# Kernel tuning notes

Measured on AMD Instinct MI355X. Metric: run time of the kernel, lower is better.

Reference implementation:

```python
import jax, jax.numpy as jnp
import numpy as np

B, CIN, T, H, W = 1, 256, 64, 32, 32
A, G = 8, 8
SCALES = jnp.array([1., 2., 4., 8., 16., 32., 64., 128.], dtype=jnp.float32)
FEAT_STRIDE = 8.0
NMS_TOP_N = 100
NMS_THRESH = 0.7
MIN_SIZE = 4.0
POS_THR, NEG_THR = 0.7, 0.3
NEG_INF = -1e9


def _conv3d(x, w, b, strides):
    y = jax.lax.conv_general_dilated(
        x, w, window_strides=strides, padding=[(1, 1)] * 3,
        dimension_numbers=('NCDHW', 'OIDHW', 'NCDHW'))
    return y + b[None, :, None, None, None]


def _iou(a, b):
    # 1D interval IoU; a, b broadcastable [..., 2] = (start, end)
    inter = jnp.maximum(jnp.minimum(a[..., 1], b[..., 1]) - jnp.maximum(a[..., 0], b[..., 0]), 0.0)
    union = (a[..., 1] - a[..., 0]) + (b[..., 1] - b[..., 0]) - inter
    return inter / jnp.maximum(union, 1e-6)


def _nms(boxes, scores):
    # greedy 1D NMS: boxes [N,2], scores [N] -> top NMS_TOP_N (zero-padded)
    n = scores.shape[0]
    def step(sc, _):
        i = jnp.argmax(sc)
        s, box = sc[i], boxes[i]
        sup = (_iou(box[None], boxes) > NMS_THRESH) | (jnp.arange(n) == i)
        return jnp.where(sup, NEG_INF, sc), (box, s)
    _, (kb, ks) = jax.lax.scan(step, scores, None, length=NMS_TOP_N)
    keep = ks > NEG_INF * 0.5
    return jnp.where(keep[:, None], kb, 0.0), jnp.where(keep, ks, 0.0)


def _forward(base_feat, gt_chunks, video_len, c1w, c1b, c2w, c2b, sw, sb, dw, db):
    bsz = base_feat.shape[0]
    x = _conv3d(base_feat, c1w, c1b, (1, 2, 2))
    x = _conv3d(x, c2w, c2b, (1, 2, 2))
    feat = jnp.max(x, axis=(3, 4))                       # AdaptiveMaxPool3d((None,1,1)) -> [B,512,T]
    tlen = feat.shape[2]
    score_logit = (jnp.einsum('oc,bct->bot', sw, feat) + sb[None, :, None]).reshape(bsz, 2, A, tlen)
    delta = (jnp.einsum('oc,bct->bot', dw, feat) + db[None, :, None]).reshape(bsz, 2, A, tlen)
    prob = jax.nn.softmax(score_logit, axis=1)
    logp = jax.nn.log_softmax(score_logit, axis=1)

    # anchors: A lengths x T temporal positions, flattened as a*T + t
    anchor_len = FEAT_STRIDE * SCALES                                    # [A]
    centers = (jnp.arange(tlen, dtype=jnp.float32) + 0.5) * FEAT_STRIDE  # [T]
    a_start = centers[None, :] - anchor_len[:, None] / 2                 # [A,T]
    a_end = centers[None, :] + anchor_len[:, None] / 2
    anchors = jnp.stack([a_start, a_end], -1).reshape(-1, 2)             # [N,2]
    N = A * tlen

    # ---- proposal decode + NMS ----
    dc, dl = delta[:, 0], delta[:, 1]                                    # [B,A,T]
    pc = centers[None, None, :] + dc * anchor_len[None, :, None]
    pl = anchor_len[None, :, None] * jnp.exp(jnp.clip(dl, -10.0, 10.0))
    lim = tlen * FEAT_STRIDE
    ps = jnp.clip(pc - pl / 2, 0.0, lim)
    pe = jnp.clip(pc + pl / 2, 0.0, lim)
    boxes = jnp.stack([ps, pe], -1).reshape(bsz, N, 2)
    fg = prob[:, 1].reshape(bsz, N)
    fg = jnp.where((pe - ps).reshape(bsz, N) >= MIN_SIZE, fg, NEG_INF)
    prop_coord, prop_score = jax.vmap(_nms)(boxes, fg)

    # ---- IoU-based label assignment ----
    ious = _iou(anchors[None, :, None, :], gt_chunks[:, None, :, :])     # [B,N,G]
    max_iou = ious.max(-1)
    arg = ious.argmax(-1)                                                # [B,N]
    label = jnp.where(max_iou < NEG_THR, 0, -1)
    label = jnp.where(max_iou >= POS_THR, 1, label)
    best = ious.argmax(1)                                                # best anchor per gt [B,G]
    bidx = jnp.arange(bsz)[:, None]
    label = label.at[bidx, best].set(1)
    vl = video_len.astype(jnp.float32)[:, None]
    inside = (anchors[None, :, 0] >= 0.0) & (anchors[None, :, 1] <= vl)
    label = jnp.where(inside, label, -1)

    matched = gt_chunks[bidx, arg]                                       # [B,N,2]
    gc = (matched[..., 0] + matched[..., 1]) / 2
    gl = jnp.maximum(matched[..., 1] - matched[..., 0], 1e-6)
    ac = (anchors[:, 0] + anchors[:, 1]) / 2
    al = anchors[:, 1] - anchors[:, 0]
    reg_label = jnp.stack([(gc - ac[None]) / al[None], jnp.log(gl / al[None])], -1)
    reg_label = jax.lax.stop_gradient(reg_label)                          # targets carry no grad

    # ---- losses ----
    logp2 = logp.reshape(bsz, 2, N).transpose(0, 2, 1)                   # [B,N,2]
    lab = jnp.maximum(label, 0)
    nll = -jnp.take_along_axis(logp2, lab[..., None], axis=2)[..., 0]
    mask = (label >= 0).astype(jnp.float32)
    cls_loss = (nll * mask).sum() / jnp.maximum(mask.sum(), 1.0)

    delta2 = delta.reshape(bsz, 2, N).transpose(0, 2, 1)                 # [B,N,2]
    d = delta2 - reg_label
    sl1 = jnp.where(jnp.abs(d) < 1.0, 0.5 * d * d, jnp.abs(d) - 0.5).sum(-1)
    pos = (label == 1).astype(jnp.float32)
    reg_loss = (sl1 * pos).sum() / jnp.maximum(pos.sum(), 1.0)
    return prop_coord, prop_score, cls_loss, reg_loss


def setup_inputs() -> dict:
    key = jax.random.key(0)
    ks = jax.random.split(key, 8)
    base_feat = jax.random.normal(ks[0], (B, CIN, T, H, W), jnp.float32)
    starts = jax.random.uniform(ks[1], (B, G), minval=0.0, maxval=448.0)
    lens = jax.random.uniform(ks[2], (B, G), minval=8.0, maxval=64.0)
    gt_chunks = jnp.stack([starts, jnp.clip(starts + lens, 0.0, T * FEAT_STRIDE)], -1)
    video_len = jnp.full((B,), int(T * FEAT_STRIDE), jnp.int32)
    s = 0.02
    return dict(
        base_feat=base_feat, gt_chunks=gt_chunks, video_len=video_len,
        conv1_w=jax.random.normal(ks[3], (512, CIN, 3, 3, 3), jnp.float32) * s,
        conv1_b=jnp.zeros((512,), jnp.float32),
        conv2_w=jax.random.normal(ks[4], (512, 512, 3, 3, 3), jnp.float32) * s,
        conv2_b=jnp.zeros((512,), jnp.float32),
        score_w=jax.random.normal(ks[5], (2 * A, 512), jnp.float32) * s,
        score_b=jnp.zeros((2 * A,), jnp.float32),
        delta_w=jax.random.normal(ks[6], (2 * A, 512), jnp.float32) * s,
        delta_b=jnp.zeros((2 * A,), jnp.float32),
    )


def reference(base_feat, gt_chunks, video_len, conv1_w, conv1_b, conv2_w, conv2_b, score_w, score_b, delta_w, delta_b):
    return _forward(base_feat, gt_chunks, video_len, conv1_w, conv1_b, conv2_w, conv2_b, score_w, score_b, delta_w, delta_b)
```

## Files before the change

kernel.cpp:

```cpp
#include <hip/hip_runtime.h>

typedef __attribute__((ext_vector_type(8))) _Float16 half8;
typedef __attribute__((ext_vector_type(4))) _Float16 half4;
typedef __attribute__((ext_vector_type(4))) float floatx4;

#define DI __device__ __forceinline__

DI void gl_lds16(const void* g, void* l) {
    __builtin_amdgcn_global_load_lds(
        (__attribute__((address_space(1))) void*)(g),
        (__attribute__((address_space(3))) void*)(l), 16, 0, 0);
}


__global__ __launch_bounds__(256) void prep_split(
        const float* __restrict__ w1, _Float16* __restrict__ w1I,
        const float* __restrict__ w2, _Float16* __restrict__ w2I,
        const float* __restrict__ in, _Float16* __restrict__ oI,
        float* __restrict__ zp) {
    __shared__ float L[13824];
    const int b = blockIdx.x;
    const int tid = threadIdx.x;
    if (b == 0 && tid < 64) zp[tid] = 0.0f;
    if (b < 512) {
        const float* src = w1 + (size_t)b * 6912;
        for (int idx = tid; idx < 6912; idx += 256) L[idx] = src[idx] * 64.0f;
        __syncthreads();
        for (int c = tid; c < 864; c += 256) {
            const int tap = c >> 5, o = c & 31;
            half8 h, l;
#pragma unroll
            for (int j = 0; j < 8; ++j) {
                const float x = L[(o * 8 + j) * 27 + tap];
                const _Float16 hh = (_Float16)x;
                h[j] = hh; l[j] = (_Float16)(x - (float)hh);
            }
            const size_t off = (size_t)b * 13824 + (size_t)(tap * 8 + (o >> 2)) * 64 + (o & 3) * 8;
            *(half8*)&w1I[off] = h;
            *(half8*)&w1I[off + 32] = l;
        }
    } else if (b < 1024) {
        const float* src = w2 + (size_t)(b - 512) * 13824;
        for (int idx = tid; idx < 13824; idx += 256) L[idx] = src[idx] * 64.0f;
        __syncthreads();
        for (int c = tid; c < 1728; c += 256) {
            const int tap = c >> 6, o = c & 63;
            half8 h, l;
#pragma unroll
            for (int j = 0; j < 8; ++j) {
                const float x = L[(o * 8 + j) * 27 + tap];
                const _Float16 hh = (_Float16)x;
                h[j] = hh; l[j] = (_Float16)(x - (float)hh);
            }
            const size_t off = (size_t)(b - 512) * 27648 + (size_t)(tap * 16 + (o >> 2)) * 64 + (o & 3) * 8;
            *(half8*)&w2I[off] = h;
            *(half8*)&w2I[off + 32] = l;
        }
    } else {
        const int idx = b - 1024;
        const int hb = idx & 1;
        const int s0 = (idx >> 1) * 64;
        const int cil = tid >> 1, part = tid & 1;
        const float* src = in + (size_t)(hb * 128 + cil) * 65536 + s0 + part * 32;
        float v[32];
#pragma unroll
        for (int q = 0; q < 8; ++q) *(float4*)(v + q * 4) = *(const float4*)(src + q * 4);
#pragma unroll
        for (int j = 0; j < 32; ++j) L[cil * 65 + part * 32 + j] = v[j];
        __syncthreads();
#pragma unroll
        for (int k = 0; k < 4; ++k) {
            const int c = tid + k * 256;
            const int sp = c >> 4, ol = c & 15;
            half8 h, l;
#pragma unroll
            for (int j = 0; j < 8; ++j) {
                const float x = L[(ol * 8 + j) * 65 + sp];
                const _Float16 hh = (_Float16)x;
                h[j] = hh; l[j] = (_Float16)(x - (float)hh);
            }
            const int og = hb * 16 + ol;
            const size_t off = (size_t)(s0 + sp) * 512 + (size_t)(og >> 2) * 64 + (og & 3) * 8;
            *(half8*)&oI[off] = h;
            *(half8*)&oI[off + 32] = l;
        }
    }
}

__global__ __launch_bounds__(256, 2) void conv1_mfma(
        const _Float16* __restrict__ xI, const _Float16* __restrict__ wI,
        const float* __restrict__ b1, const _Float16* __restrict__ zp,
        _Float16* __restrict__ yI) {
    __shared__ __align__(16) _Float16 A2[2][128 * 64];
    __shared__ __align__(16) _Float16 B3[3][128 * 64];
    const int tid = threadIdx.x;
    const int n_ = blockIdx.x;
    const int t = ((n_ & 7) << 3) | ((n_ >> 3) & 7);
    const int co_blk = (n_ >> 6) & 3;
    const int h0 = ((n_ >> 8) & 1) * 8;
    const int wid = tid >> 6, lane = tid & 63;
    const int wm = wid & 1, wn = wid >> 1;
    const int ml = lane & 15, ql = lane >> 4;
    const int cs0 = (ql ^ (ml & 7)) * 8;
    const int cs1 = ((4 + ql) ^ (ml & 7)) * 8;
    const int sl = lane & 7, rl = lane >> 3;
    const int lc = sl ^ rl;

    const _Float16* wA[4]; const _Float16* bB[4];
    int dstq[4]; bool hok[4], wok[4];
    const size_t wbo = (size_t)co_blk * 128 * 13824;
#pragma unroll
    for (int q = 0; q < 4; ++q) {
        const int row = (q * 4 + wid) * 8 + rl;
        wA[q] = wI + wbo + (size_t)row * 13824 + lc * 8;
        dstq[q] = (q * 4 + wid) * 512 + lane * 8;
        const int h = h0 + (row >> 4), w = row & 15;
        const int ih2 = 2 * h - 1, iw2 = 2 * w - 1;
        hok[q] = (ih2 >= 0); wok[q] = (iw2 >= 0);
        bB[q] = xI + (ptrdiff_t)(ih2 * 32 + iw2) * 512 + lc * 8;
    }
    const _Float16* zpl = zp + lc * 8;

    floatx4 zz = {0.f, 0.f, 0.f, 0.f};
    floatx4 acc[4][4];
#pragma unroll
    for (int i = 0; i < 4; ++i)
#pragma unroll
        for (int j = 0; j < 4; ++j) acc[i][j] = zz;

    auto stageA = [&](int kt, int cb, int KH, int KW, _Float16* Ad) {
        const size_t ab = (size_t)(((kt * 9 + KH * 3 + KW) * 8 + cb) * 64);
#pragma unroll
        for (int q = 0; q < 4; ++q) gl_lds16(wA[q] + ab, &Ad[dstq[q]]);
    };
    auto stageB = [&](int kt, int cb, int KH, int KW, _Float16* Bd) {
        const int it = t + kt - 1;
        const bool tok = ((unsigned)it < 64u);
        const ptrdiff_t boff = (ptrdiff_t)it * 524288 + KH * 16384 + KW * 512 + cb * 64;
#pragma unroll
        for (int q = 0; q < 4; ++q) {
            const bool ok = tok && (KH > 0 || hok[q]) && (KW > 0 || wok[q]);
            gl_lds16(ok ? (bB[q] + boff) : zpl, &Bd[dstq[q]]);
        }
    };

    stageA(0, 0, 0, 0, A2[0]);
    stageB(0, 0, 0, 0, B3[0]);
    stageB(0, 0, 0, 1, B3[1]);
    asm volatile("s_waitcnt vmcnt(4)" ::: "memory");
    __builtin_amdgcn_s_barrier();

    for (int o = 0; o < 24; ++o) {
        const int cb = o / 3, kt = o - cb * 3;
        const int o1 = o + 1;
        const int cb1 = o1 / 3, kt1 = o1 - cb1 * 3;
#pragma unroll
        for (int j = 0; j < 9; ++j) {
            const int par = (o + j) & 1;
            if (j < 8) stageA(kt, cb, (j + 1) / 3, (j + 1) % 3, A2[par ^ 1]);
            else       stageA(kt1, cb1, 0, 0, A2[par ^ 1]);
            if (j < 7)       stageB(kt, cb, (j + 2) / 3, (j + 2) % 3, B3[(j + 2) % 3]);
            else if (j == 7) stageB(kt1, cb1, 0, 0, B3[0]);
            else             stageB(kt1, cb1, 0, 1, B3[1]);

            const _Float16* Ab = A2[par];
            const _Float16* Bb = B3[j % 3];
            half8 ah[4], alo[4], bh8[4], blo[4];
#pragma unroll
            for (int mi = 0; mi < 4; ++mi) {
                ah[mi]  = *(const half8*)&Ab[(wm * 64 + mi * 16 + ml) * 64 + cs0];
                alo[mi] = *(const half8*)&Ab[(wm * 64 + mi * 16 + ml) * 64 + cs1];
            }
#pragma unroll
            for (int ni = 0; ni < 4; ++ni) {
                bh8[ni] = *(const half8*)&Bb[(wn * 64 + ni * 16 + ml) * 64 + cs0];
                blo[ni] = *(const half8*)&Bb[(wn * 64 + ni * 16 + ml) * 64 + cs1];
            }
            __builtin_amdgcn_s_setprio(1);
#pragma unroll
            for (int mi = 0; mi < 4; ++mi)
#pragma unroll
                for (int ni = 0; ni < 4; ++ni) {
                    acc[mi][ni] = __builtin_amdgcn_mfma_f32_16x16x32_f16(ah[mi],  bh8[ni], acc[mi][ni], 0, 0, 0);
                    acc[mi][ni] = __builtin_amdgcn_mfma_f32_16x16x32_f16(ah[mi],  blo[ni], acc[mi][ni], 0, 0, 0);
                    acc[mi][ni] = __builtin_amdgcn_mfma_f32_16x16x32_f16(alo[mi], bh8[ni], acc[mi][ni], 0, 0, 0);
                }
            __builtin_amdgcn_s_setprio(0);
            asm volatile("s_waitcnt vmcnt(4)" ::: "memory");
            __builtin_amdgcn_s_barrier();
        }
    }

    const int qr = ql * 4;
#pragma unroll
    for (int mi = 0; mi < 4; ++mi) {
        const int co = co_blk * 128 + wm * 64 + mi * 16 + qr;
#pragma unroll
        for (int ni = 0; ni < 4; ++ni) {
            const int n = wn * 64 + ni * 16 + ml;
            const int h = h0 + (n >> 4), w = n & 15;
            const size_t base = ((size_t)t * 256 + h * 16 + w) * 1024
                              + (size_t)(co >> 5) * 64 + (co & 31);
            half4 hv, lv;
#pragma unroll
            for (int r = 0; r < 4; ++r) {
                const float v = acc[mi][ni][r] * 0.015625f + b1[co + r];
                const _Float16 hb = (_Float16)v;
                hv[r] = hb;
                lv[r] = (_Float16)(v - (float)hb);
            }
            *(half4*)(yI + base) = hv;
            *(half4*)(yI + base + 32) = lv;
        }
    }
}

__global__ __launch_bounds__(256, 2) void conv2_mfma(
        const _Float16* __restrict__ xI, const _Float16* __restrict__ wI,
        const _Float16* __restrict__ zp,
        float* __restrict__ x2p) {
    __shared__ __align__(16) _Float16 A2[2][128 * 64];
    __shared__ __align__(16) _Float16 B3[3][128 * 64];
    const int tid = threadIdx.x;
    const int n_ = blockIdx.x;
    const int tp = ((n_ & 7) << 2) | ((n_ >> 3) & 3);
    const int co_blk = (n_ >> 5) & 3;
    const int ks = (n_ >> 7) & 3;
    const int wid = tid >> 6, lane = tid & 63;
    const int wm = wid & 1, wn = wid >> 1;
    const int ml = lane & 15, ql = lane >> 4;
    const int cs0 = (ql ^ (ml & 7)) * 8;
    const int cs1 = ((4 + ql) ^ (ml & 7)) * 8;
    const int sl = lane & 7, rl = lane >> 3;
    const int lc = sl ^ rl;

    const _Float16* wA[4]; const _Float16* bB[4];
    int dstq[4], itv[4]; bool hok[4], wok[4];
    const size_t wbo = (size_t)co_blk * 128 * 27648;
#pragma unroll
    for (int q = 0; q < 4; ++q) {
        const int row = (q * 4 + wid) * 8 + rl;
        wA[q] = wI + wbo + (size_t)row * 27648 + lc * 8;
        dstq[q] = (q * 4 + wid) * 512 + lane * 8;
        const int sp = row & 63;
        itv[q] = tp * 2 + (row >> 6) - 1;
        const int ih2 = 2 * (sp >> 3) - 1, iw2 = 2 * (sp & 7) - 1;
        hok[q] = (ih2 >= 0); wok[q] = (iw2 >= 0);
        bB[q] = xI + (ptrdiff_t)((itv[q] * 256 + ih2 * 16 + iw2) * 1024) + lc * 8;
    }
    const _Float16* zpl = zp + lc * 8;

    floatx4 zz = {0.f, 0.f, 0.f, 0.f};
    floatx4 acc[4][4];
#pragma unroll
    for (int i = 0; i < 4; ++i)
#pragma unroll
        for (int j = 0; j < 4; ++j) acc[i][j] = zz;

    auto stageA = [&](int kt, int cb, int KH, int KW, _Float16* Ad) {
        const size_t ab = (size_t)(((kt * 9 + KH * 3 + KW) * 16 + cb) * 64);
#pragma unroll
        for (int q = 0; q < 4; ++q) gl_lds16(wA[q] + ab, &Ad[dstq[q]]);
    };
    auto stageB = [&](int kt, int cb, int KH, int KW, _Float16* Bd) {
        const ptrdiff_t boff = (ptrdiff_t)kt * 262144 + KH * 16384 + KW * 1024 + cb * 64;
#pragma unroll
        for (int q = 0; q < 4; ++q) {
            const bool ok = ((unsigned)(itv[q] + kt) < 64u)
                         && (KH > 0 || hok[q]) && (KW > 0 || wok[q]);
            gl_lds16(ok ? (bB[q] + boff) : zpl, &Bd[dstq[q]]);
        }
    };

    stageA(0, ks * 4, 0, 0, A2[0]);
    stageB(0, ks * 4, 0, 0, B3[0]);
    stageB(0, ks * 4, 0, 1, B3[1]);
    asm volatile("s_waitcnt vmcnt(4)" ::: "memory");
    __builtin_amdgcn_s_barrier();

    for (int o = 0; o < 12; ++o) {
        const int kt = o % 3, cb = ks * 4 + o / 3;
        const int o1 = o + 1;
        const int kt1 = o1 % 3, cb1 = ks * 4 + o1 / 3;
#pragma unroll
        for (int j = 0; j < 9; ++j) {
            const int par = (o + j) & 1;
            if (j < 8) stageA(kt, cb, (j + 1) / 3, (j + 1) % 3, A2[par ^ 1]);
            else       stageA(kt1, cb1, 0, 0, A2[par ^ 1]);
            if (j < 7)       stageB(kt, cb, (j + 2) / 3, (j + 2) % 3, B3[(j + 2) % 3]);
            else if (j == 7) stageB(kt1, cb1, 0, 0, B3[0]);
            else             stageB(kt1, cb1, 0, 1, B3[1]);

            const _Float16* Ab = A2[par];
            const _Float16* Bb = B3[j % 3];
            half8 ah[4], alo[4], bh8[4], blo[4];
#pragma unroll
            for (int mi = 0; mi < 4; ++mi) {
                ah[mi]  = *(const half8*)&Ab[(wm * 64 + mi * 16 + ml) * 64 + cs0];
                alo[mi] = *(const half8*)&Ab[(wm * 64 + mi * 16 + ml) * 64 + cs1];
            }
#pragma unroll
            for (int ni = 0; ni < 4; ++ni) {
                bh8[ni] = *(const half8*)&Bb[(wn * 64 + ni * 16 + ml) * 64 + cs0];
                blo[ni] = *(const half8*)&Bb[(wn * 64 + ni * 16 + ml) * 64 + cs1];
            }
            __builtin_amdgcn_s_setprio(1);
#pragma unroll
            for (int mi = 0; mi < 4; ++mi)
#pragma unroll
                for (int ni = 0; ni < 4; ++ni) {
                    acc[mi][ni] = __builtin_amdgcn_mfma_f32_16x16x32_f16(ah[mi],  bh8[ni], acc[mi][ni], 0, 0, 0);
                    acc[mi][ni] = __builtin_amdgcn_mfma_f32_16x16x32_f16(ah[mi],  blo[ni], acc[mi][ni], 0, 0, 0);
                    acc[mi][ni] = __builtin_amdgcn_mfma_f32_16x16x32_f16(alo[mi], bh8[ni], acc[mi][ni], 0, 0, 0);
                }
            __builtin_amdgcn_s_setprio(0);
            asm volatile("s_waitcnt vmcnt(4)" ::: "memory");
            __builtin_amdgcn_s_barrier();
        }
    }

    const int qr = ql * 4;
#pragma unroll
    for (int mi = 0; mi < 4; ++mi) {
        const int co = co_blk * 128 + wm * 64 + mi * 16 + qr;
#pragma unroll
        for (int ni = 0; ni < 4; ++ni) {
            const int n = wn * 64 + ni * 16 + ml;
            const int ng = tp * 128 + n;
            float4 v;
            v.x = acc[mi][ni][0]; v.y = acc[mi][ni][1];
            v.z = acc[mi][ni][2]; v.w = acc[mi][ni][3];
            *(float4*)&x2p[((size_t)ks * 4096 + ng) * 512 + co] = v;
        }
    }
}

__global__ __launch_bounds__(256) void feat_head(
        const float* __restrict__ x2p, const float* __restrict__ b2,
        const float* __restrict__ sw, const float* __restrict__ sb,
        const float* __restrict__ dw, const float* __restrict__ db,
        float* __restrict__ scoreL, float* __restrict__ deltaL) {
    __shared__ float fr[512];
    __shared__ float partial[32][8];
    const int t = blockIdx.x, tid = threadIdx.x;
#pragma unroll
    for (int cc = 0; cc < 2; ++cc) {
        const int c = tid + cc * 256;
        float mx = -3.4e38f;
        for (int sp = 0; sp < 64; ++sp) {
            const size_t ng = (size_t)t * 64 + sp;
            const float s = x2p[ng * 512 + c]
                          + x2p[((size_t)4096 + ng) * 512 + c]
                          + x2p[((size_t)8192 + ng) * 512 + c]
                          + x2p[((size_t)12288 + ng) * 512 + c];
            mx = fmaxf(mx, s);
        }
        fr[c] = mx * 0.015625f + b2[c];
    }
    __syncthreads();
    const int o = tid & 31, part = tid >> 5;
    const float* wrow = (o < 16) ? (sw + (size_t)o * 512) : (dw + (size_t)(o - 16) * 512);
    float s = 0.f;
    const int j0 = part * 64;
#pragma unroll 16
    for (int j = 0; j < 64; ++j) s += wrow[j0 + j] * fr[j0 + j];
    partial[o][part] = s;
    __syncthreads();
    if (tid < 32) {
        float tot = 0.f;
#pragma unroll
        for (int p = 0; p < 8; ++p) tot += partial[tid][p];
        tot += (tid < 16) ? sb[tid] : db[tid - 16];
        if (tid < 16) scoreL[tid * 64 + t] = tot;
        else deltaL[(tid - 16) * 64 + t] = tot;
    }
}

__global__ void nms_loss_kernel(const float* __restrict__ scoreL,
                                const float* __restrict__ deltaL,
                                const float* __restrict__ gt,
                                const int* __restrict__ video_len,
                                float* __restrict__ out) {
    const int lane = threadIdx.x & 63;
    float gsv[8], gev[8];
#pragma unroll
    for (int g = 0; g < 8; ++g) { gsv[g] = gt[2 * g]; gev[g] = gt[2 * g + 1]; }
    const float center = ((float)lane + 0.5f) * 8.0f;
    float psv[8], pev[8], fg[8], l0v[8], l1v[8], dcv[8], dlv[8];
#pragma unroll
    for (int j = 0; j < 8; ++j) {
        const float s0 = scoreL[j * 64 + lane], s1 = scoreL[(8 + j) * 64 + lane];
        const float mm = fmaxf(s0, s1);
        const float lse = mm + logf(expf(s0 - mm) + expf(s1 - mm));
        l0v[j] = s0 - lse; l1v[j] = s1 - lse;
        const float dc = deltaL[j * 64 + lane], dl = deltaL[(8 + j) * 64 + lane];
        dcv[j] = dc; dlv[j] = dl;
        const float alen = 8.0f * (float)(1 << j);
        const float pc = center + dc * alen;
        const float pl = alen * expf(fminf(fmaxf(dl, -10.0f), 10.0f));
        const float ps = fminf(fmaxf(pc - pl * 0.5f, 0.0f), 512.0f);
        const float pe = fminf(fmaxf(pc + pl * 0.5f, 0.0f), 512.0f);
        psv[j] = ps; pev[j] = pe;
        fg[j] = ((pe - ps) >= 4.0f) ? expf(l1v[j]) : -1e9f;
    }
    for (int itn = 0; itn < 100; ++itn) {
        float v = fg[0]; int idx = lane;
#pragma unroll
        for (int j = 1; j < 8; ++j) if (fg[j] > v) { v = fg[j]; idx = lane + 64 * j; }
#pragma unroll
        for (int off = 32; off > 0; off >>= 1) {
            const float ov = __shfl_down(v, off);
            const int oi = __shfl_down(idx, off);
            if (ov > v || (ov == v && oi < idx)) { v = ov; idx = oi; }
        }
        v = __shfl(v, 0); idx = __shfl(idx, 0);
        const int wj = idx >> 6, wl = idx & 63;
        float bw0 = 0.f, bw1 = 0.f;
#pragma unroll
        for (int j = 0; j < 8; ++j) if (j == wj) { bw0 = psv[j]; bw1 = pev[j]; }
        const float b0 = __shfl(bw0, wl);
        const float b1 = __shfl(bw1, wl);
        if (lane == 0) {
            const bool kept = v > -5e8f;
            out[2 * itn] = kept ? b0 : 0.0f;
            out[2 * itn + 1] = kept ? b1 : 0.0f;
            out[200 + itn] = kept ? v : 0.0f;
        }
#pragma unroll
        for (int j = 0; j < 8; ++j) {
            const int n = lane + 64 * j;
            const float inter = fmaxf(fminf(b1, pev[j]) - fmaxf(b0, psv[j]), 0.0f);
            const float uni = (b1 - b0) + (pev[j] - psv[j]) - inter;
            const float iou = inter / fmaxf(uni, 1e-6f);
            if (iou > 0.7f || n == idx) fg[j] = -1e9f;
        }
    }
    int labv[8], aggv[8];
#pragma unroll
    for (int j = 0; j < 8; ++j) {
        const float alen = 8.0f * (float)(1 << j);
        const float as_ = center - alen * 0.5f, ae_ = center + alen * 0.5f;
        float mx = -1.0f; int ag = 0;
#pragma unroll
        for (int g = 0; g < 8; ++g) {
            const float inter = fmaxf(fminf(ae_, gev[g]) - fmaxf(as_, gsv[g]), 0.0f);
            const float uni = (ae_ - as_) + (gev[g] - gsv[g]) - inter;
            const float iou = inter / fmaxf(uni, 1e-6f);
            if (iou > mx) { mx = iou; ag = g; }
        }
        labv[j] = (mx < 0.3f) ? 0 : ((mx >= 0.7f) ? 1 : -1);
        aggv[j] = ag;
    }
    for (int g = 0; g < 8; ++g) {
        float v = -1.0f; int idx = 0;
#pragma unroll
        for (int j = 0; j < 8; ++j) {
            const int n = lane + 64 * j;
            const float alen = 8.0f * (float)(1 << j);
            const float as_ = center - alen * 0.5f, ae_ = center + alen * 0.5f;
            const float inter = fmaxf(fminf(ae_, gev[g]) - fmaxf(as_, gsv[g]), 0.0f);
            const float uni = (ae_ - as_) + (gev[g] - gsv[g]) - inter;
            const float iou = inter / fmaxf(uni, 1e-6f);
            if (iou > v || (iou == v && n < idx)) { v = iou; idx = n; }
        }
#pragma unroll
        for (int off = 32; off > 0; off >>= 1) {
            const float ov = __shfl_down(v, off);
            const int oi = __shfl_down(idx, off);
            if (ov > v || (ov == v && oi < idx)) { v = ov; idx = oi; }
        }
        idx = __shfl(idx, 0);
#pragma unroll
        for (int j = 0; j < 8; ++j)
            if (lane == (idx & 63) && j == (idx >> 6)) labv[j] = 1;
    }
    const float vl = (float)video_len[0];
    float nll_s = 0.f, msk_s = 0.f, reg_s = 0.f, pos_s = 0.f;
#pragma unroll
    for (int j = 0; j < 8; ++j) {
        const float alen = 8.0f * (float)(1 << j);
        const float as_ = center - alen * 0.5f, ae_ = center + alen * 0.5f;
        int l = labv[j];
        if (!((as_ >= 0.0f) && (ae_ <= vl))) l = -1;
        if (l >= 0) {
            msk_s += 1.0f;
            nll_s -= (l == 1) ? l1v[j] : l0v[j];
            if (l == 1) {
                pos_s += 1.0f;
                float gcv = 0.f, glv = 0.f;
#pragma unroll
                for (int g = 0; g < 8; ++g)
                    if (g == aggv[j]) {
                        gcv = (gsv[g] + gev[g]) * 0.5f;
                        glv = fmaxf(gev[g] - gsv[g], 1e-6f);
                    }
                const float r0 = (gcv - center) / alen;
                const float r1 = logf(glv / alen);
                const float d0 = dcv[j] - r0, d1 = dlv[j] - r1;
                float s = (fabsf(d0) < 1.0f) ? (0.5f * d0 * d0) : (fabsf(d0) - 0.5f);
                s += (fabsf(d1) < 1.0f) ? (0.5f * d1 * d1) : (fabsf(d1) - 0.5f);
                reg_s += s;
            }
        }
    }
    float sums[4] = {nll_s, msk_s, reg_s, pos_s};
#pragma unroll
    for (int k = 0; k < 4; ++k)
#pragma unroll
        for (int off = 32; off > 0; off >>= 1) sums[k] += __shfl_down(sums[k], off);
    if (lane == 0) {
        out[300] = sums[0] / fmaxf(sums[1], 1.0f);
        out[301] = sums[2] / fmaxf(sums[3], 1.0f);
    }
}

extern "C" void kernel_launch(void* const* d_in, const int* in_sizes, int n_in,
                              void* d_out, int out_size, void* d_ws, size_t ws_size,
                              hipStream_t stream) {
    const float* base_feat = (const float*)d_in[0];
    const float* gt        = (const float*)d_in[1];
    const int*   video_len = (const int*)d_in[2];
    const float* w1        = (const float*)d_in[3];
    const float* b1        = (const float*)d_in[4];
    const float* w2        = (const float*)d_in[5];
    const float* b2        = (const float*)d_in[6];
    const float* sw        = (const float*)d_in[7];
    const float* sb        = (const float*)d_in[8];
    const float* dw        = (const float*)d_in[9];
    const float* db        = (const float*)d_in[10];

    char* ws = (char*)d_ws;
    _Float16* w1I = (_Float16*)ws;  ws += (size_t)512 * 13824 * 2;
    _Float16* w2I = (_Float16*)ws;  ws += (size_t)512 * 27648 * 2;
    _Float16* inI = (_Float16*)ws;  ws += (size_t)65536 * 512 * 2;
    _Float16* x1I = (_Float16*)ws;  ws += (size_t)16384 * 1024 * 2;
    float* scoreL = (float*)ws;     ws += (size_t)16 * 64 * 4;
    float* deltaL = (float*)ws;     ws += (size_t)16 * 64 * 4;
    float* zpage  = (float*)ws;     ws += (size_t)64 * 4;
    float* x2p = (float*)inI;

    prep_split<<<3072, 256, 0, stream>>>(w1, w1I, w2, w2I, base_feat, inI, zpage);
    conv1_mfma<<<512, 256, 0, stream>>>(inI, w1I, b1,
                                        (const _Float16*)zpage, x1I);
    conv2_mfma<<<512, 256, 0, stream>>>(x1I, w2I,
                                        (const _Float16*)zpage, x2p);
    feat_head<<<64, 256, 0, stream>>>(x2p, b2, sw, sb, dw, db, scoreL, deltaL);
    nms_loss_kernel<<<1, 64, 0, stream>>>(scoreL, deltaL, gt, video_len,
                                          (float*)d_out);
}
```

Baseline: 750.7 us.

## Double-buffer B tile and prefetch B fragments into registers after barrier

Both conv kernels replace the triple-buffered B staging (two stages ahead) with a double buffer staged one step ahead, matching A. The B fragments for the next step are read from LDS into registers right after the barrier, so they are ready before the next MFMA block. This cuts LDS footprint (more room for occupancy) but the wait changes from vmcnt(4) to vmcnt(0). Each step now waits for all outstanding global-to-LDS loads, which reduces load/compute overlap and may expose memory latency.

```diff
diff --git a/kernel.cpp b/kernel.cpp
--- a/kernel.cpp
+++ b/kernel.cpp
@@ -92,7 +92,7 @@
         const float* __restrict__ b1, const _Float16* __restrict__ zp,
         _Float16* __restrict__ yI) {
     __shared__ __align__(16) _Float16 A2[2][128 * 64];
-    __shared__ __align__(16) _Float16 B3[3][128 * 64];
+    __shared__ __align__(16) _Float16 B2[2][128 * 64];
     const int tid = threadIdx.x;
     const int n_ = blockIdx.x;
     const int t = ((n_ & 7) << 3) | ((n_ >> 3) & 7);
@@ -144,11 +144,17 @@
         }
     };
 
+    half8 bh8c[4], bloc[4];
+
     stageA(0, 0, 0, 0, A2[0]);
-    stageB(0, 0, 0, 0, B3[0]);
-    stageB(0, 0, 0, 1, B3[1]);
-    asm volatile("s_waitcnt vmcnt(4)" ::: "memory");
+    stageB(0, 0, 0, 0, B2[0]);
+    asm volatile("s_waitcnt vmcnt(0)" ::: "memory");
     __builtin_amdgcn_s_barrier();
+#pragma unroll
+    for (int ni = 0; ni < 4; ++ni) {
+        bh8c[ni] = *(const half8*)&B2[0][(wn * 64 + ni * 16 + ml) * 64 + cs0];
+        bloc[ni] = *(const half8*)&B2[0][(wn * 64 + ni * 16 + ml) * 64 + cs1];
+    }
 
     for (int o = 0; o < 24; ++o) {
         const int cb = o / 3, kt = o - cb * 3;
@@ -157,37 +163,38 @@
 #pragma unroll
         for (int j = 0; j < 9; ++j) {
             const int par = (o + j) & 1;
-            if (j < 8) stageA(kt, cb, (j + 1) / 3, (j + 1) % 3, A2[par ^ 1]);
-            else       stageA(kt1, cb1, 0, 0, A2[par ^ 1]);
-            if (j < 7)       stageB(kt, cb, (j + 2) / 3, (j + 2) % 3, B3[(j + 2) % 3]);
-            else if (j == 7) stageB(kt1, cb1, 0, 0, B3[0]);
-            else             stageB(kt1, cb1, 0, 1, B3[1]);
-
+            if (j < 8) {
+                stageA(kt, cb, (j + 1) / 3, (j + 1) % 3, A2[par ^ 1]);
+                stageB(kt, cb, (j + 1) / 3, (j + 1) % 3, B2[par ^ 1]);
+            } else {
+                stageA(kt1, cb1, 0, 0, A2[par ^ 1]);
+                stageB(kt1, cb1, 0, 0, B2[par ^ 1]);
+            }
             const _Float16* Ab = A2[par];
-            const _Float16* Bb = B3[j % 3];
-            half8 ah[4], alo[4], bh8[4], blo[4];
+            half8 ah[4], alo[4];
 #pragma unroll
             for (int mi = 0; mi < 4; ++mi) {
                 ah[mi]  = *(const half8*)&Ab[(wm * 64 + mi * 16 + ml) * 64 + cs0];
                 alo[mi] = *(const half8*)&Ab[(wm * 64 + mi * 16 + ml) * 64 + cs1];
             }
-#pragma unroll
-            for (int ni = 0; ni < 4; ++ni) {
-                bh8[ni] = *(const half8*)&Bb[(wn * 64 + ni * 16 + ml) * 64 + cs0];
-                blo[ni] = *(const half8*)&Bb[(wn * 64 + ni * 16 + ml) * 64 + cs1];
-            }
             __builtin_amdgcn_s_setprio(1);
 #pragma unroll
             for (int mi = 0; mi < 4; ++mi)
 #pragma unroll
                 for (int ni = 0; ni < 4; ++ni) {
-                    acc[mi][ni] = __builtin_amdgcn_mfma_f32_16x16x32_f16(ah[mi],  bh8[ni], acc[mi][ni], 0, 0, 0);
-                    acc[mi][ni] = __builtin_amdgcn_mfma_f32_16x16x32_f16(ah[mi],  blo[ni], acc[mi][ni], 0, 0, 0);
-                    acc[mi][ni] = __builtin_amdgcn_mfma_f32_16x16x32_f16(alo[mi], bh8[ni], acc[mi][ni], 0, 0, 0);
+                    acc[mi][ni] = __builtin_amdgcn_mfma_f32_16x16x32_f16(ah[mi],  bh8c[ni], acc[mi][ni], 0, 0, 0);
+                    acc[mi][ni] = __builtin_amdgcn_mfma_f32_16x16x32_f16(ah[mi],  bloc[ni], acc[mi][ni], 0, 0, 0);
+                    acc[mi][ni] = __builtin_amdgcn_mfma_f32_16x16x32_f16(alo[mi], bh8c[ni], acc[mi][ni], 0, 0, 0);
                 }
             __builtin_amdgcn_s_setprio(0);
-            asm volatile("s_waitcnt vmcnt(4)" ::: "memory");
+            asm volatile("s_waitcnt vmcnt(0)" ::: "memory");
             __builtin_amdgcn_s_barrier();
+            const _Float16* Bn = B2[par ^ 1];
+#pragma unroll
+            for (int ni = 0; ni < 4; ++ni) {
+                bh8c[ni] = *(const half8*)&Bn[(wn * 64 + ni * 16 + ml) * 64 + cs0];
+                bloc[ni] = *(const half8*)&Bn[(wn * 64 + ni * 16 + ml) * 64 + cs1];
+            }
         }
     }
 
@@ -220,7 +227,7 @@
         const _Float16* __restrict__ zp,
         float* __restrict__ x2p) {
     __shared__ __align__(16) _Float16 A2[2][128 * 64];
-    __shared__ __align__(16) _Float16 B3[3][128 * 64];
+    __shared__ __align__(16) _Float16 B2[2][128 * 64];
     const int tid = threadIdx.x;
     const int n_ = blockIdx.x;
     const int tp = ((n_ & 7) << 2) | ((n_ >> 3) & 3);
@@ -272,11 +279,17 @@
         }
     };
 
+    half8 bh8c[4], bloc[4];
+
     stageA(0, ks * 4, 0, 0, A2[0]);
-    stageB(0, ks * 4, 0, 0, B3[0]);
-    stageB(0, ks * 4, 0, 1, B3[1]);
-    asm volatile("s_waitcnt vmcnt(4)" ::: "memory");
+    stageB(0, ks * 4, 0, 0, B2[0]);
+    asm volatile("s_waitcnt vmcnt(0)" ::: "memory");
     __builtin_amdgcn_s_barrier();
+#pragma unroll
+    for (int ni = 0; ni < 4; ++ni) {
+        bh8c[ni] = *(const half8*)&B2[0][(wn * 64 + ni * 16 + ml) * 64 + cs0];
+        bloc[ni] = *(const half8*)&B2[0][(wn * 64 + ni * 16 + ml) * 64 + cs1];
+    }
 
     for (int o = 0; o < 12; ++o) {
         const int kt = o % 3, cb = ks * 4 + o / 3;
@@ -285,37 +298,38 @@
 #pragma unroll
         for (int j = 0; j < 9; ++j) {
             const int par = (o + j) & 1;
-            if (j < 8) stageA(kt, cb, (j + 1) / 3, (j + 1) % 3, A2[par ^ 1]);
-            else       stageA(kt1, cb1, 0, 0, A2[par ^ 1]);
-            if (j < 7)       stageB(kt, cb, (j + 2) / 3, (j + 2) % 3, B3[(j + 2) % 3]);
-            else if (j == 7) stageB(kt1, cb1, 0, 0, B3[0]);
-            else             stageB(kt1, cb1, 0, 1, B3[1]);
-
+            if (j < 8) {
+                stageA(kt, cb, (j + 1) / 3, (j + 1) % 3, A2[par ^ 1]);
+                stageB(kt, cb, (j + 1) / 3, (j + 1) % 3, B2[par ^ 1]);
+            } else {
+                stageA(kt1, cb1, 0, 0, A2[par ^ 1]);
+                stageB(kt1, cb1, 0, 0, B2[par ^ 1]);
+            }
             const _Float16* Ab = A2[par];
-            const _Float16* Bb = B3[j % 3];
-            half8 ah[4], alo[4], bh8[4], blo[4];
+            half8 ah[4], alo[4];
 #pragma unroll
             for (int mi = 0; mi < 4; ++mi) {
                 ah[mi]  = *(const half8*)&Ab[(wm * 64 + mi * 16 + ml) * 64 + cs0];
                 alo[mi] = *(const half8*)&Ab[(wm * 64 + mi * 16 + ml) * 64 + cs1];
             }
-#pragma unroll
-            for (int ni = 0; ni < 4; ++ni) {
-                bh8[ni] = *(const half8*)&Bb[(wn * 64 + ni * 16 + ml) * 64 + cs0];
-                blo[ni] = *(const half8*)&Bb[(wn * 64 + ni * 16 + ml) * 64 + cs1];
-            }
             __builtin_amdgcn_s_setprio(1);
 #pragma unroll
             for (int mi = 0; mi < 4; ++mi)
 #pragma unroll
                 for (int ni = 0; ni < 4; ++ni) {
-                    acc[mi][ni] = __builtin_amdgcn_mfma_f32_16x16x32_f16(ah[mi],  bh8[ni], acc[mi][ni], 0, 0, 0);
-                    acc[mi][ni] = __builtin_amdgcn_mfma_f32_16x16x32_f16(ah[mi],  blo[ni], acc[mi][ni], 0, 0, 0);
-                    acc[mi][ni] = __builtin_amdgcn_mfma_f32_16x16x32_f16(alo[mi], bh8[ni], acc[mi][ni], 0, 0, 0);
+                    acc[mi][ni] = __builtin_amdgcn_mfma_f32_16x16x32_f16(ah[mi],  bh8c[ni], acc[mi][ni], 0, 0, 0);
+                    acc[mi][ni] = __builtin_amdgcn_mfma_f32_16x16x32_f16(ah[mi],  bloc[ni], acc[mi][ni], 0, 0, 0);
+                    acc[mi][ni] = __builtin_amdgcn_mfma_f32_16x16x32_f16(alo[mi], bh8c[ni], acc[mi][ni], 0, 0, 0);
                 }
             __builtin_amdgcn_s_setprio(0);
-            asm volatile("s_waitcnt vmcnt(4)" ::: "memory");
+            asm volatile("s_waitcnt vmcnt(0)" ::: "memory");
             __builtin_amdgcn_s_barrier();
+            const _Float16* Bn = B2[par ^ 1];
+#pragma unroll
+            for (int ni = 0; ni < 4; ++ni) {
+                bh8c[ni] = *(const half8*)&Bn[(wn * 64 + ni * 16 + ml) * 64 + cs0];
+                bloc[ni] = *(const half8*)&Bn[(wn * 64 + ni * 16 + ml) * 64 + cs1];
+            }
         }
     }
 
```

Result: faster. 729.5 us (median of 2 runs) (-2.8%).
